# Optimization experiments

Hardware: AMD Instinct MI355X
Metric: run time of the kernel (lower is better)

Reference implementation:

```python
import jax, jax.numpy as jnp
import numpy as np

NUM_GRAPHS = 128

def setup_inputs() -> dict:
    key = jax.random.key(0)
    ks = jax.random.split(key, 12)
    N, E = 50000, 800000
    x = jax.random.normal(ks[0], (N, 54), dtype=jnp.float32)
    edge_index = jax.random.randint(ks[1], (2, E), 0, N, dtype=jnp.int64)
    batch = jnp.sort(jax.random.randint(ks[2], (N,), 0, NUM_GRAPHS, dtype=jnp.int64))
    def lin(k, fi, fo):
        return jax.random.normal(k, (fi, fo), dtype=jnp.float32) / np.sqrt(fi)
    return {
        "x": x, "edge_index": edge_index, "batch": batch,
        "W1l": lin(ks[3], 54, 128), "b1": jnp.zeros((128,), jnp.float32), "W1r": lin(ks[4], 54, 128),
        "W2l": lin(ks[5], 128, 256), "b2": jnp.zeros((256,), jnp.float32), "W2r": lin(ks[6], 128, 256),
        "W3l": lin(ks[7], 256, 256), "b3": jnp.zeros((256,), jnp.float32), "W3r": lin(ks[8], 256, 256),
    }

def _sage(h, src, dst, n, Wl, b, Wr):
    # sum-aggregate neighbor features x_j (j=src) into node i (i=dst), then
    # out = lin_l(agg) + lin_r(h)  (PyG SAGEConv, aggr='sum')
    agg = jax.ops.segment_sum(h[src], dst, num_segments=n)
    return jax.nn.relu(agg @ Wl + b + h @ Wr)

def reference(x, edge_index, batch, W1l, b1, W1r, W2l, b2, W2r, W3l, b3, W3r):
    n = x.shape[0]
    src, dst = edge_index[0], edge_index[1]
    h = _sage(x, src, dst, n, W1l, b1, W1r)
    h = _sage(h, src, dst, n, W2l, b2, W2r)
    h = _sage(h, src, dst, n, W3l, b3, W3r)
    # global mean pool per graph (gep = global_mean_pool)
    sums = jax.ops.segment_sum(h, batch, num_segments=NUM_GRAPHS)
    cnts = jax.ops.segment_sum(jnp.ones((n, 1), h.dtype), batch, num_segments=NUM_GRAPHS)
    return sums / jnp.maximum(cnts, 1.0)
```

## Files before the change

### kernel.cpp

```cpp
#include <hip/hip_runtime.h>


typedef unsigned short u16;
typedef __attribute__((ext_vector_type(8))) short bf16x8;
typedef __attribute__((ext_vector_type(4))) float f32x4;

__device__ __forceinline__ u16 f2b(float f) {
    union { float f; unsigned u; } v; v.f = f;
    unsigned u = v.u;
    return (u16)((u + 0x7FFF + ((u >> 16) & 1)) >> 16);
}
__device__ __forceinline__ float b2f(u16 h) {
    union { unsigned u; float f; } v; v.u = ((unsigned)h) << 16;
    return v.f;
}
__device__ __forceinline__ float blo(unsigned u) {
    union { unsigned u; float f; } v; v.u = u << 16;
    return v.f;
}
__device__ __forceinline__ float bhi(unsigned u) {
    union { unsigned u; float f; } v; v.u = u & 0xffff0000u;
    return v.f;
}

__global__ void k_prep(const float* __restrict__ x,
                       const float* __restrict__ W1l, const float* __restrict__ W1r,
                       const float* __restrict__ W2l, const float* __restrict__ W2r,
                       const float* __restrict__ W3l, const float* __restrict__ W3r,
                       const int* __restrict__ dst, int* __restrict__ cntdeg,
                       u16* __restrict__ xb,
                       u16* __restrict__ wt1l, u16* __restrict__ wt1r,
                       u16* __restrict__ wt2l, u16* __restrict__ wt2r,
                       u16* __restrict__ wt3l, u16* __restrict__ wt3r,
                       int N, int E) {
    long idx = (long)blockIdx.x * 256 + threadIdx.x;
    long s0 = (long)N * 64;
    if (idx < s0) {
        int row = (int)(idx >> 6), k = (int)(idx & 63);
        xb[idx] = (k < 54) ? f2b(x[(size_t)row * 54 + k]) : 0;
        return;
    }
    idx -= s0;
    if (idx < 2 * 128 * 64) {
        u16* o = (idx < 128 * 64) ? wt1l : wt1r;
        const float* w = (idx < 128 * 64) ? W1l : W1r;
        long loc = idx % (128 * 64);
        int d = (int)(loc >> 6), k = (int)(loc & 63);
        o[loc] = (k < 54) ? f2b(w[(long)k * 128 + d]) : 0;
        return;
    }
    idx -= 2 * 128 * 64;
    if (idx < 2 * 256 * 128) {
        u16* o = (idx < 256 * 128) ? wt2l : wt2r;
        const float* w = (idx < 256 * 128) ? W2l : W2r;
        long loc = idx % (256 * 128);
        int d = (int)(loc >> 7), k = (int)(loc & 127);
        o[loc] = f2b(w[(long)k * 256 + d]);
        return;
    }
    idx -= 2 * 256 * 128;
    if (idx < 2 * 256 * 256) {
        u16* o = (idx < 256 * 256) ? wt3l : wt3r;
        const float* w = (idx < 256 * 256) ? W3l : W3r;
        long loc = idx % (256 * 256);
        int d = (int)(loc >> 8), k = (int)(loc & 255);
        o[loc] = f2b(w[(long)k * 256 + d]);
        return;
    }
    idx -= 2 * 256 * 256;
    if (idx < E) atomicAdd(&cntdeg[dst[idx]], 1);
}

__global__ void k_bsum(const int* __restrict__ cnt, int* __restrict__ bsum, int N) {
    __shared__ int sm[256];
    int i = blockIdx.x * 256 + threadIdx.x;
    sm[threadIdx.x] = (i < N) ? cnt[i] : 0;
    __syncthreads();
    for (int off = 128; off > 0; off >>= 1) {
        if (threadIdx.x < off) sm[threadIdx.x] += sm[threadIdx.x + off];
        __syncthreads();
    }
    if (threadIdx.x == 0) bsum[blockIdx.x] = sm[0];
}

__global__ void k_bscan(const int* __restrict__ bsum, int* __restrict__ boff, int NB) {
    __shared__ int sm[256];
    int t = threadIdx.x;
    int v = (t < NB) ? bsum[t] : 0;
    sm[t] = v;
    __syncthreads();
    for (int off = 1; off < 256; off <<= 1) {
        int add = (t >= off) ? sm[t - off] : 0;
        __syncthreads();
        sm[t] += add;
        __syncthreads();
    }
    if (t < NB) boff[t] = sm[t] - v;
}

__global__ void k_scan(const int* __restrict__ cnt, const int* __restrict__ boff,
                       int* __restrict__ rowptr, int* __restrict__ wpos, int N, int E) {
    __shared__ int sm[256];
    int t = threadIdx.x;
    int i = blockIdx.x * 256 + t;
    int v = (i < N) ? cnt[i] : 0;
    sm[t] = v;
    __syncthreads();
    for (int off = 1; off < 256; off <<= 1) {
        int add = (t >= off) ? sm[t - off] : 0;
        __syncthreads();
        sm[t] += add;
        __syncthreads();
    }
    int ex = sm[t] - v + boff[blockIdx.x];
    if (i < N) { rowptr[i] = ex; wpos[i] = ex; }
    if (i == 0) rowptr[N] = E;
}

template <typename TI>
__global__ void k_fill(const int* __restrict__ src, const int* __restrict__ dst,
                       int* __restrict__ wpos, TI* __restrict__ csr, int E) {
    int e = blockIdx.x * 256 + threadIdx.x;
    if (e < E) {
        int p = atomicAdd(&wpos[dst[e]], 1);
        __builtin_nontemporal_store((TI)src[e], &csr[p]);
    }
}

template <int D, int EPW, typename TI>
__global__ __launch_bounds__(256) void k_aggv(const u16* __restrict__ h,
                                              const int* __restrict__ rowptr,
                                              const TI* __restrict__ csr,
                                              u16* __restrict__ agg, int n) {
    constexpr int GRP = 64 / EPW;
    static_assert(D == GRP * 8, "geometry");
    int w = threadIdx.x >> 6;
    int lane = threadIdx.x & 63;
    int i = blockIdx.x * 4 + w;
    if (i >= n) return;
    int b0 = rowptr[i], b1 = rowptr[i + 1];
    int sub = lane / GRP;
    int dl = lane % GRP;

    float a0 = 0.f, a1 = 0.f, a2 = 0.f, a3 = 0.f;
    float a4 = 0.f, a5 = 0.f, a6 = 0.f, a7 = 0.f;

    int b = b0;
    #pragma unroll 4
    for (; b + EPW <= b1; b += EPW) {
        int s = (int)csr[b + sub];
        uint4 v = *reinterpret_cast<const uint4*>(h + (size_t)s * D + dl * 8);
        a0 += blo(v.x); a1 += bhi(v.x);
        a2 += blo(v.y); a3 += bhi(v.y);
        a4 += blo(v.z); a5 += bhi(v.z);
        a6 += blo(v.w); a7 += bhi(v.w);
    }
    int rem = b1 - b;
    if (sub < rem) {
        int s = (int)csr[b + sub];
        uint4 v = *reinterpret_cast<const uint4*>(h + (size_t)s * D + dl * 8);
        a0 += blo(v.x); a1 += bhi(v.x);
        a2 += blo(v.y); a3 += bhi(v.y);
        a4 += blo(v.z); a5 += bhi(v.z);
        a6 += blo(v.w); a7 += bhi(v.w);
    }
    #pragma unroll
    for (int off = GRP; off < 64; off <<= 1) {
        a0 += __shfl_xor(a0, off, 64);
        a1 += __shfl_xor(a1, off, 64);
        a2 += __shfl_xor(a2, off, 64);
        a3 += __shfl_xor(a3, off, 64);
        a4 += __shfl_xor(a4, off, 64);
        a5 += __shfl_xor(a5, off, 64);
        a6 += __shfl_xor(a6, off, 64);
        a7 += __shfl_xor(a7, off, 64);
    }
    if (sub == 0) {
        uint4 o;
        o.x = ((unsigned)f2b(a0)) | (((unsigned)f2b(a1)) << 16);
        o.y = ((unsigned)f2b(a2)) | (((unsigned)f2b(a3)) << 16);
        o.z = ((unsigned)f2b(a4)) | (((unsigned)f2b(a5)) << 16);
        o.w = ((unsigned)f2b(a6)) | (((unsigned)f2b(a7)) << 16);
        *reinterpret_cast<uint4*>(agg + (size_t)i * D + dl * 8) = o;
    }
}

template <int KA, int KW, int DOUT, bool A16>
__global__ __launch_bounds__(256) void k_mgemm(const u16* __restrict__ A1,
                                               const u16* __restrict__ A2,
                                               const u16* __restrict__ Wt1,
                                               const u16* __restrict__ Wt2,
                                               const float* __restrict__ bias,
                                               u16* __restrict__ C, int N) {
    constexpr int BM = 128, BKP = 40;
    __shared__ u16 As[BM * BKP];
    __shared__ u16 Bs[BM * BKP];

    const int tid = threadIdx.x;
    const int w = tid >> 6, l = tid & 63;
    const int wr = w >> 1, wc = w & 1;
    const int lo = l & 15, hi = l >> 4;
    const int m0 = blockIdx.x * BM;
    const int n0 = 0;

    f32x4 acc[4][4];
    #pragma unroll
    for (int i = 0; i < 4; ++i)
        #pragma unroll
        for (int j = 0; j < 4; ++j) acc[i][j] = {0.f, 0.f, 0.f, 0.f};

    constexpr int KT = KW / 32;

    #pragma unroll
    for (int s = 0; s < 2; ++s) {
        const u16* __restrict__ Ap = s ? A2 : A1;
        const u16* __restrict__ Wp = s ? Wt2 : Wt1;
        for (int kt = 0; kt < KT; ++kt) {
            const int k0 = kt * 32;
            #pragma unroll
            for (int it = 0; it < 2; ++it) {
                int v = it * 256 + tid;
                int r = v >> 2, c = v & 3;
                uint4 val = *reinterpret_cast<const uint4*>(Wp + (size_t)(n0 + r) * KW + k0 + c * 8);
                *reinterpret_cast<uint4*>(&Bs[r * BKP + c * 8]) = val;
            }
            if constexpr (A16) {
                #pragma unroll
                for (int it = 0; it < 2; ++it) {
                    int v = it * 256 + tid;
                    int r = v >> 2, c = v & 3;
                    int m = m0 + r;
                    uint4 val = {0u, 0u, 0u, 0u};
                    if (m < N) val = *reinterpret_cast<const uint4*>(Ap + (size_t)m * KA + k0 + c * 8);
                    *reinterpret_cast<uint4*>(&As[r * BKP + c * 8]) = val;
                }
            } else {
                #pragma unroll
                for (int it = 0; it < 8; ++it) {
                    int v = it * 256 + tid;
                    int r = v >> 4, c = v & 15;
                    int m = m0 + r;
                    int k = k0 + c * 2;
                    unsigned val = 0;
                    if (m < N && k < KA)
                        val = *reinterpret_cast<const unsigned*>(Ap + (size_t)m * KA + k);
                    *reinterpret_cast<unsigned*>(&As[r * BKP + c * 2]) = val;
                }
            }
            __syncthreads();
            bf16x8 af[4], bf[4];
            #pragma unroll
            for (int f = 0; f < 4; ++f) {
                af[f] = *reinterpret_cast<const bf16x8*>(&Bs[(wc * 64 + f * 16 + lo) * BKP + hi * 8]);
                bf[f] = *reinterpret_cast<const bf16x8*>(&As[(wr * 64 + f * 16 + lo) * BKP + hi * 8]);
            }
            #pragma unroll
            for (int fm = 0; fm < 4; ++fm)
                #pragma unroll
                for (int fn = 0; fn < 4; ++fn)
                    acc[fm][fn] = __builtin_amdgcn_mfma_f32_16x16x32_bf16(af[fn], bf[fm], acc[fm][fn], 0, 0, 0);
            __syncthreads();
        }
    }
    #pragma unroll
    for (int fm = 0; fm < 4; ++fm) {
        int node = m0 + wr * 64 + fm * 16 + lo;
        if (node < N) {
            #pragma unroll
            for (int fn = 0; fn < 4; ++fn) {
                int fb = n0 + wc * 64 + fn * 16 + hi * 4;
                float4 bv = *reinterpret_cast<const float4*>(bias + fb);
                ushort4 o;
                o.x = f2b(fmaxf(acc[fm][fn][0] + bv.x, 0.f));
                o.y = f2b(fmaxf(acc[fm][fn][1] + bv.y, 0.f));
                o.z = f2b(fmaxf(acc[fm][fn][2] + bv.z, 0.f));
                o.w = f2b(fmaxf(acc[fm][fn][3] + bv.w, 0.f));
                *reinterpret_cast<ushort4*>(C + (size_t)node * DOUT + fb) = o;
            }
        }
    }
}

template <int KA, int DOUT>
__global__ __launch_bounds__(512) void k_mgemm2(const u16* __restrict__ A1,
                                                const u16* __restrict__ A2,
                                                const u16* __restrict__ Wt1,
                                                const u16* __restrict__ Wt2,
                                                const float* __restrict__ bias,
                                                u16* __restrict__ C, int N) {
    constexpr int BM = 64, BKP = 40;
    constexpr int WCOL = DOUT / 4;
    constexpr int FN = WCOL / 16;
    __shared__ u16 As[BM * BKP];
    __shared__ u16 Bs[DOUT * BKP];

    const int tid = threadIdx.x;
    const int w = tid >> 6, lane = tid & 63;
    const int wr = w >> 2, wc = w & 3;
    const int lo = lane & 15, hi = lane >> 4;
    const int m0 = blockIdx.x * BM;

    f32x4 acc[2][FN];
    #pragma unroll
    for (int i = 0; i < 2; ++i)
        #pragma unroll
        for (int j = 0; j < FN; ++j) acc[i][j] = {0.f, 0.f, 0.f, 0.f};

    constexpr int KT = KA / 32;

    #pragma unroll
    for (int s = 0; s < 2; ++s) {
        const u16* __restrict__ Ap = s ? A2 : A1;
        const u16* __restrict__ Wp = s ? Wt2 : Wt1;
        for (int kt = 0; kt < KT; ++kt) {
            const int k0 = kt * 32;
            #pragma unroll
            for (int it = 0; it < DOUT * 32 / 8 / 512; ++it) {
                int v = it * 512 + tid;
                int r = v >> 2, c = v & 3;
                uint4 val = *reinterpret_cast<const uint4*>(Wp + (size_t)r * KA + k0 + c * 8);
                *reinterpret_cast<uint4*>(&Bs[r * BKP + c * 8]) = val;
            }
            if (tid < 256) {
                int r = tid >> 2, c = tid & 3;
                int m = m0 + r;
                uint4 val = {0u, 0u, 0u, 0u};
                if (m < N) val = *reinterpret_cast<const uint4*>(Ap + (size_t)m * KA + k0 + c * 8);
                *reinterpret_cast<uint4*>(&As[r * BKP + c * 8]) = val;
            }
            __syncthreads();
            bf16x8 bfr[2];
            #pragma unroll
            for (int fm = 0; fm < 2; ++fm)
                bfr[fm] = *reinterpret_cast<const bf16x8*>(&As[(wr * 32 + fm * 16 + lo) * BKP + hi * 8]);
            #pragma unroll
            for (int fn = 0; fn < FN; ++fn) {
                bf16x8 af = *reinterpret_cast<const bf16x8*>(&Bs[(wc * WCOL + fn * 16 + lo) * BKP + hi * 8]);
                #pragma unroll
                for (int fm = 0; fm < 2; ++fm)
                    acc[fm][fn] = __builtin_amdgcn_mfma_f32_16x16x32_bf16(af, bfr[fm], acc[fm][fn], 0, 0, 0);
            }
            __syncthreads();
        }
    }
    #pragma unroll
    for (int fm = 0; fm < 2; ++fm) {
        int node = m0 + wr * 32 + fm * 16 + lo;
        if (node < N) {
            #pragma unroll
            for (int fn = 0; fn < FN; ++fn) {
                int fb = wc * WCOL + fn * 16 + hi * 4;
                float4 bv = *reinterpret_cast<const float4*>(bias + fb);
                ushort4 o;
                o.x = f2b(fmaxf(acc[fm][fn][0] + bv.x, 0.f));
                o.y = f2b(fmaxf(acc[fm][fn][1] + bv.y, 0.f));
                o.z = f2b(fmaxf(acc[fm][fn][2] + bv.z, 0.f));
                o.w = f2b(fmaxf(acc[fm][fn][3] + bv.w, 0.f));
                *reinterpret_cast<ushort4*>(C + (size_t)node * DOUT + fb) = o;
            }
        }
    }
}

template <int ROWS>
__global__ void k_pool(const u16* __restrict__ h3, const int* __restrict__ batch,
                       float* __restrict__ outsum, int* __restrict__ cnt, int N) {
    int r0 = blockIdx.x * ROWS;
    int r1 = min(r0 + ROWS, N);
    if (r0 >= N) return;
    int d = threadIdx.x;
    int cur = batch[r0];
    float s = 0.f;
    int c = 0;
    for (int i = r0; i < r1; ++i) {
        int g = batch[i];
        if (g != cur) {
            atomicAdd(&outsum[cur * 256 + d], s);
            if (d == 0) atomicAdd(&cnt[cur], c);
            s = 0.f; c = 0; cur = g;
        }
        s += b2f(h3[(size_t)i * 256 + d]);
        c++;
    }
    atomicAdd(&outsum[cur * 256 + d], s);
    if (d == 0) atomicAdd(&cnt[cur], c);
}

__global__ void k_div(float* __restrict__ out, const int* __restrict__ cnt, int total) {
    int idx = blockIdx.x * 256 + threadIdx.x;
    if (idx < total) {
        float c = fmaxf((float)cnt[idx >> 8], 1.0f);
        out[idx] = out[idx] / c;
    }
}

extern "C" void kernel_launch(void* const* d_in, const int* in_sizes, int n_in,
                              void* d_out, int out_size, void* d_ws, size_t ws_size,
                              hipStream_t stream) {
    const float* x   = (const float*)d_in[0];
    const int* ei    = (const int*)d_in[1];
    const int* batch = (const int*)d_in[2];
    const float* W1l = (const float*)d_in[3];
    const float* b1  = (const float*)d_in[4];
    const float* W1r = (const float*)d_in[5];
    const float* W2l = (const float*)d_in[6];
    const float* b2  = (const float*)d_in[7];
    const float* W2r = (const float*)d_in[8];
    const float* W3l = (const float*)d_in[9];
    const float* b3  = (const float*)d_in[10];
    const float* W3r = (const float*)d_in[11];

    const int N = in_sizes[0] / 54;
    const int E = in_sizes[1] / 2;
    const int* src = ei;
    const int* dst = ei + E;

    u16* xb   = (u16*)d_ws;
    u16* bufA = xb + (size_t)N * 64;
    u16* buf1 = bufA + (size_t)N * 256;
    u16* buf2 = buf1 + (size_t)N * 256;
    u16* wt1l = buf2 + (size_t)N * 256;
    u16* wt1r = wt1l + 128 * 64;
    u16* wt2l = wt1r + 128 * 64;
    u16* wt2r = wt2l + 256 * 128;
    u16* wt3l = wt2r + 256 * 128;
    u16* wt3r = wt3l + 256 * 256;
    int* ip = (int*)(wt3r + 256 * 256);
    int* cntdeg  = ip; ip += N;
    int* rowptr  = ip; ip += N + 1;
    int* wpos    = ip; ip += N + 1;
    int* bsum    = ip; ip += 256;
    int* boff    = ip; ip += 256;
    int* cntpool = ip; ip += 128;
    int* csr32   = ip;
    u16* csr16   = (u16*)csr32;

    hipMemsetAsync(cntdeg, 0, (size_t)N * sizeof(int), stream);
    hipMemsetAsync(d_out, 0, (size_t)out_size * sizeof(float), stream);
    hipMemsetAsync(cntpool, 0, 128 * sizeof(int), stream);

    const int NB = (N + 255) / 256;
    const int EB = (E + 255) / 256;

    {
        long total = (long)N * 64 + 2L * 128 * 64 + 2L * 256 * 128 + 2L * 256 * 256 + E;
        int g = (int)((total + 255) / 256);
        k_prep<<<g, 256, 0, stream>>>(x, W1l, W1r, W2l, W2r, W3l, W3r,
                                      dst, cntdeg,
                                      xb, wt1l, wt1r, wt2l, wt2r, wt3l, wt3r, N, E);
    }

    k_bsum<<<NB, 256, 0, stream>>>(cntdeg, bsum, N);
    k_bscan<<<1, 256, 0, stream>>>(bsum, boff, NB);
    k_scan<<<NB, 256, 0, stream>>>(cntdeg, boff, rowptr, wpos, N, E);

    const int AGB = (N + 3) / 4;
    const int GX = (N + 127) / 128;
    const int GX2 = (N + 63) / 64;

    if (N <= 65535) {
        k_fill<u16><<<EB, 256, 0, stream>>>(src, dst, wpos, csr16, E);
        k_aggv<64, 8, u16><<<AGB, 256, 0, stream>>>(xb, rowptr, csr16, bufA, N);
        k_mgemm<64, 64, 128, true><<<GX, 256, 0, stream>>>(bufA, xb, wt1l, wt1r, b1, buf1, N);
        k_aggv<128, 4, u16><<<AGB, 256, 0, stream>>>(buf1, rowptr, csr16, bufA, N);
        k_mgemm2<128, 256><<<GX2, 512, 0, stream>>>(bufA, buf1, wt2l, wt2r, b2, buf2, N);
        k_aggv<256, 2, u16><<<AGB, 256, 0, stream>>>(buf2, rowptr, csr16, bufA, N);
        k_mgemm2<256, 256><<<GX2, 512, 0, stream>>>(bufA, buf2, wt3l, wt3r, b3, buf1, N);
    } else {
        k_fill<int><<<EB, 256, 0, stream>>>(src, dst, wpos, csr32, E);
        k_aggv<64, 8, int><<<AGB, 256, 0, stream>>>(xb, rowptr, csr32, bufA, N);
        k_mgemm<64, 64, 128, true><<<GX, 256, 0, stream>>>(bufA, xb, wt1l, wt1r, b1, buf1, N);
        k_aggv<128, 4, int><<<AGB, 256, 0, stream>>>(buf1, rowptr, csr32, bufA, N);
        k_mgemm2<128, 256><<<GX2, 512, 0, stream>>>(bufA, buf1, wt2l, wt2r, b2, buf2, N);
        k_aggv<256, 2, int><<<AGB, 256, 0, stream>>>(buf2, rowptr, csr32, bufA, N);
        k_mgemm2<256, 256><<<GX2, 512, 0, stream>>>(bufA, buf2, wt3l, wt3r, b3, buf1, N);
    }

    k_pool<32><<<(N + 31) / 32, 256, 0, stream>>>(buf1, batch, (float*)d_out, cntpool, N);
    k_div<<<(out_size + 255) / 256, 256, 0, stream>>>((float*)d_out, cntpool, out_size);
}
```

Measured before the change: 312.0 us.

## Build CSR via two-pass bucket partition with LDS-local atomics

Replaces the single scatter-with-global-atomics CSR fill with a two-pass scheme. Edges are first partitioned into buckets of 64 destination nodes, packed as src|dst<<16 in a 32-bit word. A per-bucket block then scatters them using shared-memory atomics into the final u16 CSR. The aim is to cut contention on random per-node global atomics and scattered 2-byte stores, at the cost of an extra kernel launch and an extra pass over E packed words.

```diff
diff --git a/kernel.cpp b/kernel.cpp
--- a/kernel.cpp
+++ b/kernel.cpp
@@ -2,6 +2,7 @@
 
 
 typedef unsigned short u16;
+typedef unsigned int u32;
 typedef __attribute__((ext_vector_type(8))) short bf16x8;
 typedef __attribute__((ext_vector_type(4))) float f32x4;
 
@@ -117,13 +118,51 @@
     if (i == 0) rowptr[N] = E;
 }
 
-template <typename TI>
+__global__ void k_binit(const int* __restrict__ rowptr, int* __restrict__ bucketpos,
+                        int B, int N) {
+    int b = blockIdx.x * 256 + threadIdx.x;
+    if (b < B) {
+        int n0 = b << 6;
+        bucketpos[b] = rowptr[n0 > N ? N : n0];
+    }
+}
+
+__global__ void k_part(const int* __restrict__ src, const int* __restrict__ dst,
+                       int* __restrict__ bucketpos, u32* __restrict__ ebuf, int E) {
+    int e = blockIdx.x * 256 + threadIdx.x;
+    if (e < E) {
+        int d = dst[e];
+        int p = atomicAdd(&bucketpos[d >> 6], 1);
+        ebuf[p] = (u32)src[e] | ((u32)d << 16);
+    }
+}
+
+__global__ __launch_bounds__(256) void k_fill2(const int* __restrict__ rowptr,
+                                               const u32* __restrict__ ebuf,
+                                               u16* __restrict__ csr, int N) {
+    __shared__ int lwpos[64];
+    int b = blockIdx.x;
+    int node0 = b << 6;
+    int node1 = min(node0 + 64, N);
+    int t = threadIdx.x;
+    if (t < 64) lwpos[t] = (node0 + t < node1) ? rowptr[node0 + t] : 0;
+    __syncthreads();
+    int e0 = rowptr[node0];
+    int e1 = rowptr[node1];
+    for (int e = e0 + t; e < e1; e += 256) {
+        u32 v = ebuf[e];
+        int li = (int)(v >> 16) - node0;
+        int pos = atomicAdd(&lwpos[li], 1);
+        csr[pos] = (u16)(v & 0xffffu);
+    }
+}
+
 __global__ void k_fill(const int* __restrict__ src, const int* __restrict__ dst,
-                       int* __restrict__ wpos, TI* __restrict__ csr, int E) {
+                       int* __restrict__ wpos, int* __restrict__ csr, int E) {
     int e = blockIdx.x * 256 + threadIdx.x;
     if (e < E) {
         int p = atomicAdd(&wpos[dst[e]], 1);
-        __builtin_nontemporal_store((TI)src[e], &csr[p]);
+        csr[p] = src[e];
     }
 }
 
@@ -432,7 +471,9 @@
     int* bsum    = ip; ip += 256;
     int* boff    = ip; ip += 256;
     int* cntpool = ip; ip += 128;
-    int* csr32   = ip;
+    int* bucketpos = ip; ip += 1024;
+    int* csr32   = ip; ip += E;
+    u32* ebuf    = (u32*)ip;
     u16* csr16   = (u16*)csr32;
 
     hipMemsetAsync(cntdeg, 0, (size_t)N * sizeof(int), stream);
@@ -459,7 +500,11 @@
     const int GX2 = (N + 63) / 64;
 
     if (N <= 65535) {
-        k_fill<u16><<<EB, 256, 0, stream>>>(src, dst, wpos, csr16, E);
+        const int B = (N + 63) >> 6;
+        k_binit<<<(B + 255) / 256, 256, 0, stream>>>(rowptr, bucketpos, B, N);
+        k_part<<<EB, 256, 0, stream>>>(src, dst, bucketpos, ebuf, E);
+        k_fill2<<<B, 256, 0, stream>>>(rowptr, ebuf, csr16, N);
+
         k_aggv<64, 8, u16><<<AGB, 256, 0, stream>>>(xb, rowptr, csr16, bufA, N);
         k_mgemm<64, 64, 128, true><<<GX, 256, 0, stream>>>(bufA, xb, wt1l, wt1r, b1, buf1, N);
         k_aggv<128, 4, u16><<<AGB, 256, 0, stream>>>(buf1, rowptr, csr16, bufA, N);
@@ -467,7 +512,7 @@
         k_aggv<256, 2, u16><<<AGB, 256, 0, stream>>>(buf2, rowptr, csr16, bufA, N);
         k_mgemm2<256, 256><<<GX2, 512, 0, stream>>>(bufA, buf2, wt3l, wt3r, b3, buf1, N);
     } else {
-        k_fill<int><<<EB, 256, 0, stream>>>(src, dst, wpos, csr32, E);
+        k_fill<<<EB, 256, 0, stream>>>(src, dst, wpos, csr32, E);
         k_aggv<64, 8, int><<<AGB, 256, 0, stream>>>(xb, rowptr, csr32, bufA, N);
         k_mgemm<64, 64, 128, true><<<GX, 256, 0, stream>>>(bufA, xb, wt1l, wt1r, b1, buf1, N);
         k_aggv<128, 4, int><<<AGB, 256, 0, stream>>>(buf1, rowptr, csr32, bufA, N);
```

Measured after the change: 461.4 us. 47.9% more time.
